# Kernel optimization log

Hardware: AMD Instinct MI355X
Metric: run time of the kernel (lower is better)

## Reference

```python
import jax, jax.numpy as jnp
import numpy as np

NUM_HEADS = 16
D_MODEL = 1024


def setup_inputs() -> dict:
    key = jax.random.key(0)
    ks = jax.random.split(key, 12)
    B, S, D = 2, 2048, D_MODEL
    scale = 1.0 / np.sqrt(D)
    inp = {
        "query": jax.random.normal(ks[0], (B, S, D), dtype=jnp.float32),
        "key": jax.random.normal(ks[1], (B, S, D), dtype=jnp.float32),
        "value": jax.random.normal(ks[2], (B, S, D), dtype=jnp.float32),
        "mask": jax.random.randint(ks[3], (B, S, S), 0, 2, dtype=jnp.int32),
        # four Linear(d_model, d_model) layers: torch layout W [out, in], y = x @ W.T + b
        "Wq": jax.random.normal(ks[4], (D, D), dtype=jnp.float32) * scale,
        "bq": jnp.zeros((D,), dtype=jnp.float32),
        "Wk": jax.random.normal(ks[5], (D, D), dtype=jnp.float32) * scale,
        "bk": jnp.zeros((D,), dtype=jnp.float32),
        "Wv": jax.random.normal(ks[6], (D, D), dtype=jnp.float32) * scale,
        "bv": jnp.zeros((D,), dtype=jnp.float32),
        "Wo": jax.random.normal(ks[7], (D, D), dtype=jnp.float32) * scale,
        "bo": jnp.zeros((D,), dtype=jnp.float32),
    }
    return inp


def reference(query, key, value, mask, Wq, bq, Wk, bk, Wv, bv, Wo, bo):
    B, S, D = query.shape
    H = NUM_HEADS
    dk = D // H

    def split_heads(x):  # [B,S,D] -> [B,H,S,dk]
        return x.reshape(B, S, H, dk).transpose(0, 2, 1, 3)

    q = split_heads(query @ Wq.T + bq)
    k = split_heads(key @ Wk.T + bk)
    v = split_heads(value @ Wv.T + bv)

    # naive full-score attention, faithful to the original
    scores = jnp.einsum("bhqd,bhkd->bhqk", q, k) / jnp.sqrt(jnp.asarray(dk, q.dtype))
    scores = jnp.where(mask[:, None, :, :] == 0, jnp.asarray(-1e9, scores.dtype), scores)
    probs = jax.nn.softmax(scores, axis=-1)
    attn = jnp.einsum("bhqk,bhkd->bhqd", probs, v)  # [B,H,S,dk]

    out = attn.transpose(0, 2, 1, 3).reshape(B, S, D)
    return out @ Wo.T + bo
```

## Files before the change

kernel.cpp:

```cpp
#include <hip/hip_runtime.h>
#include <hip/hip_bf16.h>

#define NH 16
#define DK 64
#define SEQ 2048
#define DMODEL 1024
#define BATCH 2
#define MROWS (BATCH * SEQ)

using bf16x8 = __attribute__((ext_vector_type(8))) short;
using f32x4  = __attribute__((ext_vector_type(4))) float;

#define NEGI (-1e30f)
#define QSCALE 0.18033688f

static __device__ __forceinline__ unsigned short f2bf(float x) {
  unsigned u = __builtin_bit_cast(unsigned, x);
  u += 0x7fffu + ((u >> 16) & 1u);
  return (unsigned short)(u >> 16);
}
static __device__ __forceinline__ float bf2f(unsigned short h) {
  unsigned u = ((unsigned)h) << 16;
  return __builtin_bit_cast(float, u);
}
static __device__ __forceinline__ unsigned cvtpk(float a, float b) {
  unsigned r;
  asm("v_cvt_pk_bf16_f32 %0, %1, %2" : "=v"(r) : "v"(a), "v"(b));
  return r;
}

__global__ __launch_bounds__(256) void convert3(const float* __restrict__ s0,
                                                const float* __restrict__ s1,
                                                const float* __restrict__ s2,
                                                unsigned short* __restrict__ d0,
                                                unsigned short* __restrict__ d1,
                                                unsigned short* __restrict__ d2,
                                                long n8, int blkseg) {
  int seg = blockIdx.x / blkseg;
  int ib  = blockIdx.x % blkseg;
  const float* s = seg == 0 ? s0 : (seg == 1 ? s1 : s2);
  unsigned short* d = seg == 0 ? d0 : (seg == 1 ? d1 : d2);
  long i0 = (long)ib * blockDim.x + threadIdx.x;
  long stride = (long)blkseg * blockDim.x;
  for (long i = i0; i < n8; i += stride) {
    const float* p = s + i * 8;
    float4 a = *(const float4*)(p);
    float4 b = *(const float4*)(p + 4);
    bf16x8 v;
    v[0] = (short)f2bf(a.x); v[1] = (short)f2bf(a.y);
    v[2] = (short)f2bf(a.z); v[3] = (short)f2bf(a.w);
    v[4] = (short)f2bf(b.x); v[5] = (short)f2bf(b.y);
    v[6] = (short)f2bf(b.z); v[7] = (short)f2bf(b.w);
    *(bf16x8*)(d + i * 8) = v;
  }
}
__global__ __launch_bounds__(256) void convert4(const float* __restrict__ s0,
                                                const float* __restrict__ s1,
                                                const float* __restrict__ s2,
                                                const float* __restrict__ s3,
                                                unsigned short* __restrict__ d0,
                                                unsigned short* __restrict__ d1,
                                                unsigned short* __restrict__ d2,
                                                unsigned short* __restrict__ d3,
                                                long n8, int blkseg) {
  int seg = blockIdx.x / blkseg;
  int ib  = blockIdx.x % blkseg;
  const float* s = seg == 0 ? s0 : (seg == 1 ? s1 : (seg == 2 ? s2 : s3));
  unsigned short* d = seg == 0 ? d0 : (seg == 1 ? d1 : (seg == 2 ? d2 : d3));
  long i0 = (long)ib * blockDim.x + threadIdx.x;
  long stride = (long)blkseg * blockDim.x;
  for (long i = i0; i < n8; i += stride) {
    const float* p = s + i * 8;
    float4 a = *(const float4*)(p);
    float4 b = *(const float4*)(p + 4);
    bf16x8 v;
    v[0] = (short)f2bf(a.x); v[1] = (short)f2bf(a.y);
    v[2] = (short)f2bf(a.z); v[3] = (short)f2bf(a.w);
    v[4] = (short)f2bf(b.x); v[5] = (short)f2bf(b.y);
    v[6] = (short)f2bf(b.z); v[7] = (short)f2bf(b.w);
    *(bf16x8*)(d + i * 8) = v;
  }
}

__global__ __launch_bounds__(256) void pack_mask(const int* __restrict__ mask,
                                                 unsigned long long* __restrict__ pm,
                                                 int nwords) {
  int wid  = (blockIdx.x * blockDim.x + threadIdx.x) >> 6;
  int lane = threadIdx.x & 63;
  int nw   = (gridDim.x * blockDim.x) >> 6;
  for (int w = wid; w < nwords; w += nw) {
    int v = mask[(long)w * 64 + lane];
    unsigned long long b = __ballot(v != 0);
    if (lane == 0) pm[w] = b;
  }
}

#define BK 64
#define LDA2 72

static __device__ __forceinline__ void gemm_body(const unsigned short* __restrict__ A,
                                                 const unsigned short* __restrict__ W,
                                                 const unsigned short* __restrict__ bias,
                                                 void* __restrict__ Cv,
                                                 int mode, float cscale, int bid,
                                                 unsigned short* Al, unsigned short* Bl) {
  const int t    = threadIdx.x;
  const int lane = t & 63;
  const int w    = t >> 6;
  const int wm   = w >> 1, wn = w & 1;
  const int g    = lane >> 4, lr = lane & 15;
  const int nb   = bid & 7;
  const int mb   = bid >> 3;
  const long Abase = (long)mb * 128 * 1024;
  const long Wbase = (long)nb * 128 * 1024;

  f32x4 acc[4][4] = {};

  for (int kt = 0; kt < 1024; kt += BK) {
    __syncthreads();
#pragma unroll
    for (int q = 0; q < 4; ++q) {
      int id  = q * 256 + t;
      int row = id >> 3;
      int c8  = (id & 7) << 3;
      bf16x8 va = *(const bf16x8*)(A + Abase + (long)row * 1024 + kt + c8);
      bf16x8 vb = *(const bf16x8*)(W + Wbase + (long)row * 1024 + kt + c8);
      *(bf16x8*)(&Al[row * LDA2 + c8]) = va;
      *(bf16x8*)(&Bl[row * LDA2 + c8]) = vb;
    }
    __syncthreads();
#pragma unroll
    for (int kh = 0; kh < 2; ++kh) {
      bf16x8 af[4], bfr[4];
#pragma unroll
      for (int i = 0; i < 4; ++i) {
        af[i]  = *(const bf16x8*)(&Al[(wm * 64 + i * 16 + lr) * LDA2 + kh * 32 + g * 8]);
        bfr[i] = *(const bf16x8*)(&Bl[(wn * 64 + i * 16 + lr) * LDA2 + kh * 32 + g * 8]);
      }
#pragma unroll
      for (int i = 0; i < 4; ++i)
#pragma unroll
        for (int j = 0; j < 4; ++j)
          acc[i][j] = __builtin_amdgcn_mfma_f32_16x16x32_bf16(af[i], bfr[j], acc[i][j], 0, 0, 0);
    }
  }

#pragma unroll
  for (int j = 0; j < 4; ++j) {
    int n = nb * 128 + wn * 64 + j * 16 + lr;
    float bv = bf2f(bias[n]);
#pragma unroll
    for (int i = 0; i < 4; ++i) {
      int m0 = mb * 128 + wm * 64 + i * 16 + g * 4;
      float v0 = (acc[i][j][0] + bv) * cscale;
      float v1 = (acc[i][j][1] + bv) * cscale;
      float v2 = (acc[i][j][2] + bv) * cscale;
      float v3 = (acc[i][j][3] + bv) * cscale;
      if (mode == 2) {
        int b = m0 >> 11, s0 = m0 & (SEQ - 1);
        int h = n >> 6, d = n & (DK - 1);
        uint2 pk;
        pk.x = (unsigned)f2bf(v0) | ((unsigned)f2bf(v1) << 16);
        pk.y = (unsigned)f2bf(v2) | ((unsigned)f2bf(v3) << 16);
        *(uint2*)(&((unsigned short*)Cv)[((long)(b * NH + h) * DK + d) * SEQ + s0]) = pk;
      } else if (mode == 1) {
        int b = m0 >> 11, s0 = m0 & (SEQ - 1);
        int h = n >> 6, d = n & (DK - 1);
        unsigned short* p = &((unsigned short*)Cv)[(((long)(b * NH + h) * SEQ + s0) << 6) + d];
        p[0] = f2bf(v0); p[64] = f2bf(v1); p[128] = f2bf(v2); p[192] = f2bf(v3);
      } else {
        float* p = &((float*)Cv)[(long)m0 * DMODEL + n];
        p[0] = v0; p[DMODEL] = v1; p[2 * DMODEL] = v2; p[3 * DMODEL] = v3;
      }
    }
  }
}

__global__ __launch_bounds__(256) void qkv_proj(const unsigned short* __restrict__ Aq,
                                                const unsigned short* __restrict__ Ak,
                                                const unsigned short* __restrict__ Av,
                                                const unsigned short* __restrict__ Wq,
                                                const unsigned short* __restrict__ Wk,
                                                const unsigned short* __restrict__ Wv,
                                                const unsigned short* __restrict__ bq,
                                                const unsigned short* __restrict__ bk,
                                                const unsigned short* __restrict__ bv,
                                                unsigned short* __restrict__ Cq,
                                                unsigned short* __restrict__ Ck,
                                                unsigned short* __restrict__ Cv) {
  __shared__ unsigned short Al[128 * LDA2];
  __shared__ unsigned short Bl[128 * LDA2];
  int which = blockIdx.x >> 8;
  int bid   = blockIdx.x & 255;
  const unsigned short* A = which == 0 ? Aq : (which == 1 ? Ak : Av);
  const unsigned short* W = which == 0 ? Wq : (which == 1 ? Wk : Wv);
  const unsigned short* b = which == 0 ? bq : (which == 1 ? bk : bv);
  unsigned short* C = which == 0 ? Cq : (which == 1 ? Ck : Cv);
  int   mode  = which == 2 ? 2 : 1;
  float scale = which == 0 ? QSCALE : 1.0f;
  gemm_body(A, W, b, C, mode, scale, bid, Al, Bl);
}

__global__ __launch_bounds__(256) void gemm_out(const unsigned short* __restrict__ A,
                                                const unsigned short* __restrict__ W,
                                                const unsigned short* __restrict__ bias,
                                                float* __restrict__ C) {
  __shared__ unsigned short Al[128 * LDA2];
  __shared__ unsigned short Bl[128 * LDA2];
  gemm_body(A, W, bias, C, 0, 1.0f, blockIdx.x, Al, Bl);
}

#define KVB 64
#define LD 72

__global__ __launch_bounds__(256) void attn(const unsigned short* __restrict__ Q,
                                            const unsigned short* __restrict__ K,
                                            const unsigned short* __restrict__ VT,
                                            const unsigned long long* __restrict__ pm,
                                            unsigned short* __restrict__ O) {
  __shared__ unsigned short Kl[KVB * LD];
  __shared__ unsigned short Vt[DK * LD];
  __shared__ unsigned short Pl[4][32 * LD];
  const int t    = threadIdx.x;
  const int lane = t & 63;
  const int w    = t >> 6;
  const int g    = lane >> 4, lr = lane & 15;
  const int qb   = blockIdx.x & 15;
  const int bh   = blockIdx.x >> 4;
  const int b    = bh >> 4, h = bh & 15;
  const long base = (long)bh * SEQ * DK;
  const int q0   = qb * 128 + w * 32;

  bf16x8 qf[2][2];
#pragma unroll
  for (int qh = 0; qh < 2; ++qh) {
    const unsigned short* qp = Q + base + (long)(q0 + qh * 16 + lr) * DK;
    qf[qh][0] = *(const bf16x8*)(qp + g * 8);
    qf[qh][1] = *(const bf16x8*)(qp + 32 + g * 8);
  }
  float mrun[2] = {NEGI, NEGI}, lrun[2] = {0.f, 0.f};
  f32x4 o[2][4] = {};

  for (int kt = 0; kt < SEQ / KVB; ++kt) {
    const int kvbase = kt * KVB;
    __syncthreads();
#pragma unroll
    for (int p = 0; p < 2; ++p) {
      int id  = p * 256 + t;
      int row = id >> 3;
      int c8  = (id & 7) << 3;
      bf16x8 kv8 = *(const bf16x8*)(K + base + (long)(kvbase + row) * DK + c8);
      *(bf16x8*)(&Kl[row * LD + c8]) = kv8;
    }
#pragma unroll
    for (int p = 0; p < 2; ++p) {
      int id  = p * 256 + t;
      int row = id >> 3;
      int c8  = (id & 7) << 3;
      bf16x8 vv = *(const bf16x8*)(VT + base + (long)row * SEQ + kvbase + c8);
      *(bf16x8*)(&Vt[row * LD + c8]) = vv;
    }
    __syncthreads();

    f32x4 sc[2][4];
#pragma unroll
    for (int c = 0; c < 4; ++c) {
      bf16x8 kf0 = *(const bf16x8*)(&Kl[(c * 16 + lr) * LD + g * 8]);
      bf16x8 kf1 = *(const bf16x8*)(&Kl[(c * 16 + lr) * LD + 32 + g * 8]);
#pragma unroll
      for (int qh = 0; qh < 2; ++qh) {
        f32x4 a = {};
        a = __builtin_amdgcn_mfma_f32_16x16x32_bf16(kf0, qf[qh][0], a, 0, 0, 0);
        a = __builtin_amdgcn_mfma_f32_16x16x32_bf16(kf1, qf[qh][1], a, 0, 0, 0);
        sc[qh][c] = a;
      }
    }

    unsigned short* P = &Pl[w][0];
#pragma unroll
    for (int qh = 0; qh < 2; ++qh) {
      const unsigned long long mw = pm[((long)b * SEQ + q0 + qh * 16 + lr) * 32 + kt];
      float s[4][4];
      float mt = NEGI;
#pragma unroll
      for (int c = 0; c < 4; ++c)
#pragma unroll
        for (int r = 0; r < 4; ++r) {
          int kvi = c * 16 + g * 4 + r;
          float v = ((mw >> kvi) & 1ull) ? sc[qh][c][r] : -1e9f;
          s[c][r] = v;
          mt = fmaxf(mt, v);
        }
      mt = fmaxf(mt, __shfl_xor(mt, 16, 64));
      mt = fmaxf(mt, __shfl_xor(mt, 32, 64));

      int need = __any(mt > mrun[qh] + 5.0f);
      float mn = mrun[qh], corr = 1.0f;
      if (need) { mn = fmaxf(mrun[qh], mt); corr = __builtin_amdgcn_exp2f(mrun[qh] - mn); mrun[qh] = mn; }

      float pf[4][4];
      float rs = 0.f;
#pragma unroll
      for (int c = 0; c < 4; ++c)
#pragma unroll
        for (int r = 0; r < 4; ++r) {
          float p_ = __builtin_amdgcn_exp2f(s[c][r] - mn);
          pf[c][r] = p_;
          rs += p_;
        }
      rs += __shfl_xor(rs, 16, 64);
      rs += __shfl_xor(rs, 32, 64);

      if (need) {
        lrun[qh] = lrun[qh] * corr + rs;
#pragma unroll
        for (int r = 0; r < 4; ++r) {
          float cq = __shfl(corr, (lane >> 4) * 4 + r, 64);
#pragma unroll
          for (int dt = 0; dt < 4; ++dt) o[qh][dt][r] *= cq;
        }
      } else {
        lrun[qh] += rs;
      }

#pragma unroll
      for (int c = 0; c < 4; ++c) {
        uint2 pk;
        pk.x = cvtpk(pf[c][0], pf[c][1]);
        pk.y = cvtpk(pf[c][2], pf[c][3]);
        *(uint2*)(&P[(qh * 16 + lr) * LD + c * 16 + g * 4]) = pk;
      }
    }
    __syncthreads();
#pragma unroll
    for (int c32 = 0; c32 < 2; ++c32) {
      bf16x8 pf0 = *(const bf16x8*)(&P[lr * LD + c32 * 32 + g * 8]);
      bf16x8 pf1 = *(const bf16x8*)(&P[(16 + lr) * LD + c32 * 32 + g * 8]);
#pragma unroll
      for (int dt = 0; dt < 4; ++dt) {
        bf16x8 vf = *(const bf16x8*)(&Vt[(dt * 16 + lr) * LD + c32 * 32 + g * 8]);
        o[0][dt] = __builtin_amdgcn_mfma_f32_16x16x32_bf16(pf0, vf, o[0][dt], 0, 0, 0);
        o[1][dt] = __builtin_amdgcn_mfma_f32_16x16x32_bf16(pf1, vf, o[1][dt], 0, 0, 0);
      }
    }
  }
#pragma unroll
  for (int qh = 0; qh < 2; ++qh) {
    float inv = 1.0f / lrun[qh];
#pragma unroll
    for (int r = 0; r < 4; ++r) {
      float iq = __shfl(inv, (lane >> 4) * 4 + r, 64);
      int q = q0 + qh * 16 + g * 4 + r;
      unsigned short* op = O + ((long)(b * SEQ + q) * DMODEL) + h * DK;
#pragma unroll
      for (int dt = 0; dt < 4; ++dt) op[dt * 16 + lr] = f2bf(o[qh][dt][r] * iq);
    }
  }
}

extern "C" void kernel_launch(void* const* d_in, const int* in_sizes, int n_in,
                              void* d_out, int out_size, void* d_ws, size_t ws_size,
                              hipStream_t stream) {
  const int* maskp = (const int*)d_in[3];
  float* out = (float*)d_out;

  char* ws = (char*)d_ws;
  const long MB = 1 << 20;
  unsigned long long* pm = (unsigned long long*)ws;
  unsigned short* Qc  = (unsigned short*)(ws + 1 * MB);
  unsigned short* Kc  = (unsigned short*)(ws + 9 * MB);
  unsigned short* Vc  = (unsigned short*)(ws + 17 * MB);
  unsigned short* Wqc = (unsigned short*)(ws + 25 * MB);
  unsigned short* Wkc = (unsigned short*)(ws + 27 * MB);
  unsigned short* Wvc = (unsigned short*)(ws + 29 * MB);
  unsigned short* Woc = (unsigned short*)(ws + 31 * MB);
  unsigned short* bqc = (unsigned short*)(ws + 33 * MB);
  unsigned short* bkc = (unsigned short*)(ws + 33 * MB + 4096);
  unsigned short* bvc = (unsigned short*)(ws + 33 * MB + 8192);
  unsigned short* boc = (unsigned short*)(ws + 33 * MB + 12288);
  unsigned short* Qb  = (unsigned short*)(ws + 35 * MB);
  unsigned short* Kb  = (unsigned short*)(ws + 43 * MB);
  unsigned short* Vb  = (unsigned short*)(ws + 51 * MB);
  unsigned short* Ab  = (unsigned short*)(ws + 59 * MB);

  const long nQKV8 = (long)MROWS * DMODEL / 8;
  const long nW8   = (long)DMODEL * DMODEL / 8;
  convert3<<<1536, 256, 0, stream>>>((const float*)d_in[0], (const float*)d_in[1],
                                     (const float*)d_in[2], Qc, Kc, Vc, nQKV8, 512);
  convert4<<<512, 256, 0, stream>>>((const float*)d_in[4], (const float*)d_in[6],
                                    (const float*)d_in[8], (const float*)d_in[10],
                                    Wqc, Wkc, Wvc, Woc, nW8, 128);
  convert4<<<4, 256, 0, stream>>>((const float*)d_in[5], (const float*)d_in[7],
                                  (const float*)d_in[9], (const float*)d_in[11],
                                  bqc, bkc, bvc, boc, DMODEL / 8, 1);

  const int nwords = BATCH * SEQ * (SEQ / 64);
  pack_mask<<<512, 256, 0, stream>>>(maskp, pm, nwords);

  qkv_proj<<<768, 256, 0, stream>>>(Qc, Kc, Vc, Wqc, Wkc, Wvc,
                                    bqc, bkc, bvc, Qb, Kb, Vb);

  attn<<<BATCH * NH * (SEQ / 128), 256, 0, stream>>>(Qb, Kb, Vb, pm, Ab);

  gemm_out<<<256, 256, 0, stream>>>(Ab, Woc, boc, out);
}
```

Before: 200.2 us.

## Split attention KV range in two halves and merge partial softmax results

The attention kernel now splits the key/value sequence into two halves, so each block handles half the KV range. This doubles the grid to raise CU occupancy. Each half writes unnormalised fp32 outputs plus its running max and sum to a workspace buffer. A new merge kernel rescales and combines the two halves and writes the bf16 result. The trade is extra global traffic for the fp32 partials, an extra launch, and scalar, poorly coalesced bf16 stores in the merge.

```diff
diff --git a/kernel.cpp b/kernel.cpp
--- a/kernel.cpp
+++ b/kernel.cpp
@@ -212,12 +212,14 @@
 
 #define KVB 64
 #define LD 72
-
-__global__ __launch_bounds__(256) void attn(const unsigned short* __restrict__ Q,
-                                            const unsigned short* __restrict__ K,
-                                            const unsigned short* __restrict__ VT,
-                                            const unsigned long long* __restrict__ pm,
-                                            unsigned short* __restrict__ O) {
+#define HALF_ROWS (32L * 2048)
+
+__global__ __launch_bounds__(256) void attn_part(const unsigned short* __restrict__ Q,
+                                                 const unsigned short* __restrict__ K,
+                                                 const unsigned short* __restrict__ VT,
+                                                 const unsigned long long* __restrict__ pm,
+                                                 float* __restrict__ Obuf,
+                                                 float* __restrict__ ML) {
   __shared__ unsigned short Kl[KVB * LD];
   __shared__ unsigned short Vt[DK * LD];
   __shared__ unsigned short Pl[4][32 * LD];
@@ -225,11 +227,13 @@
   const int lane = t & 63;
   const int w    = t >> 6;
   const int g    = lane >> 4, lr = lane & 15;
-  const int qb   = blockIdx.x & 15;
-  const int bh   = blockIdx.x >> 4;
-  const int b    = bh >> 4, h = bh & 15;
+  const int half = blockIdx.x >> 9;
+  const int rest = blockIdx.x & 511;
+  const int qb   = rest & 15;
+  const int bh   = rest >> 4;
   const long base = (long)bh * SEQ * DK;
   const int q0   = qb * 128 + w * 32;
+  const int kv0  = half * (SEQ / 2);
 
   bf16x8 qf[2][2];
 #pragma unroll
@@ -241,8 +245,8 @@
   float mrun[2] = {NEGI, NEGI}, lrun[2] = {0.f, 0.f};
   f32x4 o[2][4] = {};
 
-  for (int kt = 0; kt < SEQ / KVB; ++kt) {
-    const int kvbase = kt * KVB;
+  for (int kt = 0; kt < SEQ / KVB / 2; ++kt) {
+    const int kvbase = kv0 + kt * KVB;
     __syncthreads();
 #pragma unroll
     for (int p = 0; p < 2; ++p) {
@@ -279,7 +283,8 @@
     unsigned short* P = &Pl[w][0];
 #pragma unroll
     for (int qh = 0; qh < 2; ++qh) {
-      const unsigned long long mw = pm[((long)b * SEQ + q0 + qh * 16 + lr) * 32 + kt];
+      const unsigned long long mw =
+          pm[((long)(bh >> 4) * SEQ + q0 + qh * 16 + lr) * 32 + (kvbase >> 6)];
       float s[4][4];
       float mt = NEGI;
 #pragma unroll
@@ -344,17 +349,49 @@
       }
     }
   }
+  const long rowbase = half * HALF_ROWS + (long)bh * SEQ;
 #pragma unroll
   for (int qh = 0; qh < 2; ++qh) {
-    float inv = 1.0f / lrun[qh];
 #pragma unroll
     for (int r = 0; r < 4; ++r) {
-      float iq = __shfl(inv, (lane >> 4) * 4 + r, 64);
       int q = q0 + qh * 16 + g * 4 + r;
-      unsigned short* op = O + ((long)(b * SEQ + q) * DMODEL) + h * DK;
-#pragma unroll
-      for (int dt = 0; dt < 4; ++dt) op[dt * 16 + lr] = f2bf(o[qh][dt][r] * iq);
-    }
+      float* op = Obuf + (rowbase + q) * DK;
+#pragma unroll
+      for (int dt = 0; dt < 4; ++dt) op[dt * 16 + lr] = o[qh][dt][r];
+    }
+    if (g == 0) {
+      long mi = (rowbase + q0 + qh * 16 + lr) * 2;
+      ML[mi]     = mrun[qh];
+      ML[mi + 1] = lrun[qh];
+    }
+  }
+}
+
+__global__ __launch_bounds__(256) void attn_merge(const float* __restrict__ Obuf,
+                                                  const float* __restrict__ ML,
+                                                  unsigned short* __restrict__ Ab) {
+  int tid = blockIdx.x * 256 + threadIdx.x;
+  int bh = tid >> 11, q = tid & 2047;
+  int b = bh >> 4, h = bh & 15;
+  long i1 = (long)bh * SEQ + q;
+  long i2 = HALF_ROWS + i1;
+  float m1 = ML[i1 * 2], l1 = ML[i1 * 2 + 1];
+  float m2 = ML[i2 * 2], l2 = ML[i2 * 2 + 1];
+  float ms = fmaxf(m1, m2);
+  float w1 = __builtin_amdgcn_exp2f(m1 - ms);
+  float w2 = __builtin_amdgcn_exp2f(m2 - ms);
+  float inv = 1.0f / fmaxf(l1 * w1 + l2 * w2, 1e-35f);
+  const float* O1 = Obuf + i1 * DK;
+  const float* O2 = Obuf + i2 * DK;
+  unsigned short* orow = Ab + ((long)(b * SEQ + q)) * DMODEL + h * DK;
+#pragma unroll
+  for (int d0 = 0; d0 < DK; d0 += 4) {
+    float4 a = *(const float4*)(O1 + d0);
+    float4 c = *(const float4*)(O2 + d0);
+    orow[d0 + 0] = f2bf((a.x * w1 + c.x * w2) * inv);
+    orow[d0 + 1] = f2bf((a.y * w1 + c.y * w2) * inv);
+    orow[d0 + 2] = f2bf((a.z * w1 + c.z * w2) * inv);
+    orow[d0 + 3] = f2bf((a.w * w1 + c.w * w2) * inv);
   }
 }
 
@@ -382,6 +419,8 @@
   unsigned short* Kb  = (unsigned short*)(ws + 43 * MB);
   unsigned short* Vb  = (unsigned short*)(ws + 51 * MB);
   unsigned short* Ab  = (unsigned short*)(ws + 59 * MB);
+  float*          Obuf= (float*)(ws + 67 * MB);
+  float*          MLb = (float*)(ws + 102 * MB);
 
   const long nQKV8 = (long)MROWS * DMODEL / 8;
   const long nW8   = (long)DMODEL * DMODEL / 8;
@@ -400,7 +439,8 @@
   qkv_proj<<<768, 256, 0, stream>>>(Qc, Kc, Vc, Wqc, Wkc, Wvc,
                                     bqc, bkc, bvc, Qb, Kb, Vb);
 
-  attn<<<BATCH * NH * (SEQ / 128), 256, 0, stream>>>(Qb, Kb, Vb, pm, Ab);
+  attn_part<<<2 * BATCH * NH * (SEQ / 128), 256, 0, stream>>>(Qb, Kb, Vb, pm, Obuf, MLb);
+  attn_merge<<<BATCH * NH * SEQ / 256, 256, 0, stream>>>(Obuf, MLb, Ab);
 
   gemm_out<<<256, 256, 0, stream>>>(Ab, Woc, boc, out);
 }
```

New measurement: 217.1 us. +8.5%, slower.

## Load K/V fragments directly from global memory and remap blocks per XCD

Applied to the files above, without the earlier changes.

The attention kernel stops staging K and V tiles in shared memory and instead has each wave read its MFMA operand fragments straight from global memory, relying on L2/L1 caching. This removes both per-iteration block-wide __syncthreads; the per-wave P buffer is now fenced only with lgkmcnt waits and scheduling barriers. Block indices are also remapped so that the blocks of a given batch-head land on the same XCD, which should improve L2 reuse of K/V. The trade-off is redundant global and cache traffic, since the four waves each fetch the same K/V data.

```diff
diff --git a/kernel.cpp b/kernel.cpp
--- a/kernel.cpp
+++ b/kernel.cpp
@@ -218,16 +218,16 @@
                                             const unsigned short* __restrict__ VT,
                                             const unsigned long long* __restrict__ pm,
                                             unsigned short* __restrict__ O) {
-  __shared__ unsigned short Kl[KVB * LD];
-  __shared__ unsigned short Vt[DK * LD];
   __shared__ unsigned short Pl[4][32 * LD];
   const int t    = threadIdx.x;
   const int lane = t & 63;
   const int w    = t >> 6;
   const int g    = lane >> 4, lr = lane & 15;
-  const int qb   = blockIdx.x & 15;
-  const int bh   = blockIdx.x >> 4;
-  const int b    = bh >> 4, h = bh & 15;
+  const int xcd  = blockIdx.x & 7;
+  const int idx  = blockIdx.x >> 3;
+  const int bh   = xcd * 4 + (idx >> 4);
+  const int qb   = idx & 15;
+  const int b    = bh >> 4;
   const long base = (long)bh * SEQ * DK;
   const int q0   = qb * 128 + w * 32;
 
@@ -240,33 +240,17 @@
   }
   float mrun[2] = {NEGI, NEGI}, lrun[2] = {0.f, 0.f};
   f32x4 o[2][4] = {};
+  unsigned short* P = &Pl[w][0];
 
   for (int kt = 0; kt < SEQ / KVB; ++kt) {
     const int kvbase = kt * KVB;
-    __syncthreads();
-#pragma unroll
-    for (int p = 0; p < 2; ++p) {
-      int id  = p * 256 + t;
-      int row = id >> 3;
-      int c8  = (id & 7) << 3;
-      bf16x8 kv8 = *(const bf16x8*)(K + base + (long)(kvbase + row) * DK + c8);
-      *(bf16x8*)(&Kl[row * LD + c8]) = kv8;
-    }
-#pragma unroll
-    for (int p = 0; p < 2; ++p) {
-      int id  = p * 256 + t;
-      int row = id >> 3;
-      int c8  = (id & 7) << 3;
-      bf16x8 vv = *(const bf16x8*)(VT + base + (long)row * SEQ + kvbase + c8);
-      *(bf16x8*)(&Vt[row * LD + c8]) = vv;
-    }
-    __syncthreads();
 
     f32x4 sc[2][4];
 #pragma unroll
     for (int c = 0; c < 4; ++c) {
-      bf16x8 kf0 = *(const bf16x8*)(&Kl[(c * 16 + lr) * LD + g * 8]);
-      bf16x8 kf1 = *(const bf16x8*)(&Kl[(c * 16 + lr) * LD + 32 + g * 8]);
+      const unsigned short* kp = K + base + (long)(kvbase + c * 16 + lr) * DK;
+      bf16x8 kf0 = *(const bf16x8*)(kp + g * 8);
+      bf16x8 kf1 = *(const bf16x8*)(kp + 32 + g * 8);
 #pragma unroll
       for (int qh = 0; qh < 2; ++qh) {
         f32x4 a = {};
@@ -276,7 +260,6 @@
       }
     }
 
-    unsigned short* P = &Pl[w][0];
 #pragma unroll
     for (int qh = 0; qh < 2; ++qh) {
       const unsigned long long mw = pm[((long)b * SEQ + q0 + qh * 16 + lr) * 32 + kt];
@@ -331,18 +314,23 @@
         *(uint2*)(&P[(qh * 16 + lr) * LD + c * 16 + g * 4]) = pk;
       }
     }
-    __syncthreads();
+    asm volatile("s_waitcnt lgkmcnt(0)" ::: "memory");
+    __builtin_amdgcn_sched_barrier(0);
+
 #pragma unroll
     for (int c32 = 0; c32 < 2; ++c32) {
       bf16x8 pf0 = *(const bf16x8*)(&P[lr * LD + c32 * 32 + g * 8]);
       bf16x8 pf1 = *(const bf16x8*)(&P[(16 + lr) * LD + c32 * 32 + g * 8]);
 #pragma unroll
       for (int dt = 0; dt < 4; ++dt) {
-        bf16x8 vf = *(const bf16x8*)(&Vt[(dt * 16 + lr) * LD + c32 * 32 + g * 8]);
+        bf16x8 vf = *(const bf16x8*)(VT + base + (long)(dt * 16 + lr) * SEQ
+                                     + kvbase + c32 * 32 + g * 8);
         o[0][dt] = __builtin_amdgcn_mfma_f32_16x16x32_bf16(pf0, vf, o[0][dt], 0, 0, 0);
         o[1][dt] = __builtin_amdgcn_mfma_f32_16x16x32_bf16(pf1, vf, o[1][dt], 0, 0, 0);
       }
     }
+    asm volatile("s_waitcnt lgkmcnt(0)" ::: "memory");
+    __builtin_amdgcn_sched_barrier(0);
   }
 #pragma unroll
   for (int qh = 0; qh < 2; ++qh) {
@@ -351,7 +339,7 @@
     for (int r = 0; r < 4; ++r) {
       float iq = __shfl(inv, (lane >> 4) * 4 + r, 64);
       int q = q0 + qh * 16 + g * 4 + r;
-      unsigned short* op = O + ((long)(b * SEQ + q) * DMODEL) + h * DK;
+      unsigned short* op = O + ((long)(b * SEQ + q) * DMODEL) + (bh & 15) * DK;
 #pragma unroll
       for (int dt = 0; dt < 4; ++dt) op[dt * 16 + lr] = f2bf(o[qh][dt][r] * iq);
     }
```

New measurement: 245.5 us. +22.7%, slower.

## Switch attention to 32x32x16 MFMA and keep P in registers via permlane swap

Applied to the files above, without the earlier changes.

Rewrites the attention inner loop to use 32x32x16 bf16 MFMA tiles instead of 16x16x32. With the S^T layout, the softmax probabilities can be rearranged into the A operand of the PV MFMA using permlane32_swap (or shuffles), so the per-wave LDS P buffer and the extra __syncthreads are no longer needed. This cuts LDS traffic and one barrier per KV tile, and it also simplifies the row reductions to a single cross-half shuffle. The cost is 16-wide accumulators, which raise register pressure, and a layout mapping that is harder to get right.

```diff
diff --git a/kernel.cpp b/kernel.cpp
--- a/kernel.cpp
+++ b/kernel.cpp
@@ -10,6 +10,8 @@
 
 using bf16x8 = __attribute__((ext_vector_type(8))) short;
 using f32x4  = __attribute__((ext_vector_type(4))) float;
+using f32x16 = __attribute__((ext_vector_type(16))) float;
+using i32x2  = __attribute__((ext_vector_type(2))) int;
 
 #define NEGI (-1e30f)
 #define QSCALE 0.18033688f
@@ -220,26 +222,26 @@
                                             unsigned short* __restrict__ O) {
   __shared__ unsigned short Kl[KVB * LD];
   __shared__ unsigned short Vt[DK * LD];
-  __shared__ unsigned short Pl[4][32 * LD];
   const int t    = threadIdx.x;
   const int lane = t & 63;
   const int w    = t >> 6;
-  const int g    = lane >> 4, lr = lane & 15;
+  const int ln31 = lane & 31;
+  const int hi   = lane >> 5;
   const int qb   = blockIdx.x & 15;
   const int bh   = blockIdx.x >> 4;
   const int b    = bh >> 4, h = bh & 15;
   const long base = (long)bh * SEQ * DK;
   const int q0   = qb * 128 + w * 32;
 
-  bf16x8 qf[2][2];
-#pragma unroll
-  for (int qh = 0; qh < 2; ++qh) {
-    const unsigned short* qp = Q + base + (long)(q0 + qh * 16 + lr) * DK;
-    qf[qh][0] = *(const bf16x8*)(qp + g * 8);
-    qf[qh][1] = *(const bf16x8*)(qp + 32 + g * 8);
-  }
-  float mrun[2] = {NEGI, NEGI}, lrun[2] = {0.f, 0.f};
-  f32x4 o[2][4] = {};
+  bf16x8 qfr[4];
+  {
+    const unsigned short* qp = Q + base + (long)(q0 + ln31) * DK + hi * 8;
+#pragma unroll
+    for (int c = 0; c < 4; ++c) qfr[c] = *(const bf16x8*)(qp + c * 16);
+  }
+  float mrun = NEGI, lrun = 0.f;
+  f32x16 o0 = {}, o1 = {};
+  const unsigned long long* pmrow = pm + ((long)b * SEQ + q0 + ln31) * 32;
 
   for (int kt = 0; kt < SEQ / KVB; ++kt) {
     const int kvbase = kt * KVB;
@@ -249,112 +251,105 @@
       int id  = p * 256 + t;
       int row = id >> 3;
       int c8  = (id & 7) << 3;
-      bf16x8 kv8 = *(const bf16x8*)(K + base + (long)(kvbase + row) * DK + c8);
-      *(bf16x8*)(&Kl[row * LD + c8]) = kv8;
-    }
-#pragma unroll
-    for (int p = 0; p < 2; ++p) {
-      int id  = p * 256 + t;
-      int row = id >> 3;
-      int c8  = (id & 7) << 3;
-      bf16x8 vv = *(const bf16x8*)(VT + base + (long)row * SEQ + kvbase + c8);
-      *(bf16x8*)(&Vt[row * LD + c8]) = vv;
+      *(bf16x8*)(&Kl[row * LD + c8]) =
+          *(const bf16x8*)(K + base + (long)(kvbase + row) * DK + c8);
+      *(bf16x8*)(&Vt[row * LD + c8]) =
+          *(const bf16x8*)(VT + base + (long)row * SEQ + kvbase + c8);
     }
     __syncthreads();
 
-    f32x4 sc[2][4];
+    f32x16 sc0 = {}, sc1 = {};
 #pragma unroll
     for (int c = 0; c < 4; ++c) {
-      bf16x8 kf0 = *(const bf16x8*)(&Kl[(c * 16 + lr) * LD + g * 8]);
-      bf16x8 kf1 = *(const bf16x8*)(&Kl[(c * 16 + lr) * LD + 32 + g * 8]);
-#pragma unroll
-      for (int qh = 0; qh < 2; ++qh) {
-        f32x4 a = {};
-        a = __builtin_amdgcn_mfma_f32_16x16x32_bf16(kf0, qf[qh][0], a, 0, 0, 0);
-        a = __builtin_amdgcn_mfma_f32_16x16x32_bf16(kf1, qf[qh][1], a, 0, 0, 0);
-        sc[qh][c] = a;
+      bf16x8 kf0 = *(const bf16x8*)(&Kl[ln31 * LD + c * 16 + hi * 8]);
+      bf16x8 kf1 = *(const bf16x8*)(&Kl[(32 + ln31) * LD + c * 16 + hi * 8]);
+      sc0 = __builtin_amdgcn_mfma_f32_32x32x16_bf16(kf0, qfr[c], sc0, 0, 0, 0);
+      sc1 = __builtin_amdgcn_mfma_f32_32x32x16_bf16(kf1, qfr[c], sc1, 0, 0, 0);
+    }
+
+    const unsigned long long mw = pmrow[kt];
+    float mt = NEGI;
+#pragma unroll
+    for (int r = 0; r < 16; ++r) {
+      int kvl = (r & 3) + 8 * (r >> 2) + 4 * hi;
+      float v0 = ((mw >> kvl) & 1ull) ? sc0[r] : -1e9f;
+      float v1 = ((mw >> (32 + kvl)) & 1ull) ? sc1[r] : -1e9f;
+      sc0[r] = v0; sc1[r] = v1;
+      mt = fmaxf(mt, fmaxf(v0, v1));
+    }
+    mt = fmaxf(mt, __shfl_xor(mt, 32, 64));
+
+    int need = __any(mt > mrun + 5.0f);
+    float mn = mrun, corr = 1.0f;
+    if (need) { mn = fmaxf(mrun, mt); corr = __builtin_amdgcn_exp2f(mrun - mn); mrun = mn; }
+
+    float rs = 0.f;
+#pragma unroll
+    for (int r = 0; r < 16; ++r) {
+      sc0[r] = __builtin_amdgcn_exp2f(sc0[r] - mn);
+      sc1[r] = __builtin_amdgcn_exp2f(sc1[r] - mn);
+      rs += sc0[r] + sc1[r];
+    }
+    rs += __shfl_xor(rs, 32, 64);
+
+    if (need) {
+      lrun = lrun * corr + rs;
+#pragma unroll
+      for (int r = 0; r < 16; ++r) {
+        int qq = (r & 3) + 8 * (r >> 2) + 4 * hi;
+        float cq = __shfl(corr, qq, 64);
+        o0[r] *= cq; o1[r] *= cq;
       }
-    }
-
-    unsigned short* P = &Pl[w][0];
-#pragma unroll
-    for (int qh = 0; qh < 2; ++qh) {
-      const unsigned long long mw = pm[((long)b * SEQ + q0 + qh * 16 + lr) * 32 + kt];
-      float s[4][4];
-      float mt = NEGI;
-#pragma unroll
-      for (int c = 0; c < 4; ++c)
-#pragma unroll
-        for (int r = 0; r < 4; ++r) {
-          int kvi = c * 16 + g * 4 + r;
-          float v = ((mw >> kvi) & 1ull) ? sc[qh][c][r] : -1e9f;
-          s[c][r] = v;
-          mt = fmaxf(mt, v);
-        }
-      mt = fmaxf(mt, __shfl_xor(mt, 16, 64));
-      mt = fmaxf(mt, __shfl_xor(mt, 32, 64));
-
-      int need = __any(mt > mrun[qh] + 5.0f);
-      float mn = mrun[qh], corr = 1.0f;
-      if (need) { mn = fmaxf(mrun[qh], mt); corr = __builtin_amdgcn_exp2f(mrun[qh] - mn); mrun[qh] = mn; }
-
-      float pf[4][4];
-      float rs = 0.f;
-#pragma unroll
-      for (int c = 0; c < 4; ++c)
-#pragma unroll
-        for (int r = 0; r < 4; ++r) {
-          float p_ = __builtin_amdgcn_exp2f(s[c][r] - mn);
-          pf[c][r] = p_;
-          rs += p_;
-        }
-      rs += __shfl_xor(rs, 16, 64);
-      rs += __shfl_xor(rs, 32, 64);
-
-      if (need) {
-        lrun[qh] = lrun[qh] * corr + rs;
-#pragma unroll
-        for (int r = 0; r < 4; ++r) {
-          float cq = __shfl(corr, (lane >> 4) * 4 + r, 64);
-#pragma unroll
-          for (int dt = 0; dt < 4; ++dt) o[qh][dt][r] *= cq;
-        }
-      } else {
-        lrun[qh] += rs;
+    } else {
+      lrun += rs;
+    }
+
+    bf16x8 pa[4];
+#pragma unroll
+    for (int sub = 0; sub < 2; ++sub) {
+      unsigned wv[8];
+#pragma unroll
+      for (int j = 0; j < 8; ++j) {
+        float a  = (sub == 0) ? sc0[2 * j]     : sc1[2 * j];
+        float c_ = (sub == 0) ? sc0[2 * j + 1] : sc1[2 * j + 1];
+        wv[j] = cvtpk(a, c_);
       }
-
-#pragma unroll
-      for (int c = 0; c < 4; ++c) {
-        uint2 pk;
-        pk.x = cvtpk(pf[c][0], pf[c][1]);
-        pk.y = cvtpk(pf[c][2], pf[c][3]);
-        *(uint2*)(&P[(qh * 16 + lr) * LD + c * 16 + g * 4]) = pk;
-      }
-    }
-    __syncthreads();
-#pragma unroll
-    for (int c32 = 0; c32 < 2; ++c32) {
-      bf16x8 pf0 = *(const bf16x8*)(&P[lr * LD + c32 * 32 + g * 8]);
-      bf16x8 pf1 = *(const bf16x8*)(&P[(16 + lr) * LD + c32 * 32 + g * 8]);
-#pragma unroll
-      for (int dt = 0; dt < 4; ++dt) {
-        bf16x8 vf = *(const bf16x8*)(&Vt[(dt * 16 + lr) * LD + c32 * 32 + g * 8]);
-        o[0][dt] = __builtin_amdgcn_mfma_f32_16x16x32_bf16(pf0, vf, o[0][dt], 0, 0, 0);
-        o[1][dt] = __builtin_amdgcn_mfma_f32_16x16x32_bf16(pf1, vf, o[1][dt], 0, 0, 0);
-      }
-    }
-  }
-#pragma unroll
-  for (int qh = 0; qh < 2; ++qh) {
-    float inv = 1.0f / lrun[qh];
-#pragma unroll
-    for (int r = 0; r < 4; ++r) {
-      float iq = __shfl(inv, (lane >> 4) * 4 + r, 64);
-      int q = q0 + qh * 16 + g * 4 + r;
-      unsigned short* op = O + ((long)(b * SEQ + q) * DMODEL) + h * DK;
-#pragma unroll
-      for (int dt = 0; dt < 4; ++dt) op[dt * 16 + lr] = f2bf(o[qh][dt][r] * iq);
-    }
+#if __has_builtin(__builtin_amdgcn_permlane32_swap)
+      i32x2 sA = __builtin_amdgcn_permlane32_swap((int)wv[0], (int)wv[2], false, false);
+      i32x2 sB = __builtin_amdgcn_permlane32_swap((int)wv[1], (int)wv[3], false, false);
+      i32x2 sC = __builtin_amdgcn_permlane32_swap((int)wv[4], (int)wv[6], false, false);
+      i32x2 sD = __builtin_amdgcn_permlane32_swap((int)wv[5], (int)wv[7], false, false);
+      uint4 f0 = {(unsigned)sA.x, (unsigned)sB.x, (unsigned)sA.y, (unsigned)sB.y};
+      uint4 f1 = {(unsigned)sC.x, (unsigned)sD.x, (unsigned)sC.y, (unsigned)sD.y};
+#else
+      unsigned x0 = __shfl_xor(wv[0], 32, 64), x1 = __shfl_xor(wv[1], 32, 64);
+      unsigned x2 = __shfl_xor(wv[2], 32, 64), x3 = __shfl_xor(wv[3], 32, 64);
+      unsigned x4 = __shfl_xor(wv[4], 32, 64), x5 = __shfl_xor(wv[5], 32, 64);
+      unsigned x6 = __shfl_xor(wv[6], 32, 64), x7 = __shfl_xor(wv[7], 32, 64);
+      uint4 f0 = {hi ? x2 : wv[0], hi ? x3 : wv[1], hi ? wv[2] : x0, hi ? wv[3] : x1};
+      uint4 f1 = {hi ? x6 : wv[4], hi ? x7 : wv[5], hi ? wv[6] : x4, hi ? wv[7] : x5};
+#endif
+      pa[sub * 2]     = __builtin_bit_cast(bf16x8, f0);
+      pa[sub * 2 + 1] = __builtin_bit_cast(bf16x8, f1);
+    }
+
+#pragma unroll
+    for (int c = 0; c < 4; ++c) {
+      bf16x8 vf0 = *(const bf16x8*)(&Vt[ln31 * LD + c * 16 + hi * 8]);
+      bf16x8 vf1 = *(const bf16x8*)(&Vt[(32 + ln31) * LD + c * 16 + hi * 8]);
+      o0 = __builtin_amdgcn_mfma_f32_32x32x16_bf16(pa[c], vf0, o0, 0, 0, 0);
+      o1 = __builtin_amdgcn_mfma_f32_32x32x16_bf16(pa[c], vf1, o1, 0, 0, 0);
+    }
+  }
+
+  float inv = 1.0f / lrun;
+#pragma unroll
+  for (int r = 0; r < 16; ++r) {
+    int qq = (r & 3) + 8 * (r >> 2) + 4 * hi;
+    float iq = __shfl(inv, qq, 64);
+    unsigned short* op = O + ((long)(b * SEQ + q0 + qq) * DMODEL) + h * DK + ln31;
+    op[0]  = f2bf(o0[r] * iq);
+    op[32] = f2bf(o1[r] * iq);
   }
 }
 
```

Result: slower. 221.4 us (+10.6%).
